# Optimization experiments

Hardware: AMD Instinct MI355X
Metric: run time of the kernel (lower is better)

The kernel has to match this reference:

```python
import jax, jax.numpy as jnp
import numpy as np

D_FEATURES = 64
N_DEPTH = 2048
N_HEAD = 8
N_CHANNEL = 2
N_VCHANNEL = 2
BATCH = 4


def setup_inputs() -> dict:
    key = jax.random.key(0)
    ks = jax.random.split(key, 7)
    F = D_FEATURES
    qk_out = N_HEAD * N_CHANNEL * F   # 1024
    v_out = N_HEAD * N_VCHANNEL * F   # 1024
    # xavier-normal-ish init for expansion (pointwise linear) weights
    def xavier(k, fan_in, fan_out):
        std = float(np.sqrt(2.0 / (fan_in + fan_out)))
        return jax.random.normal(k, (fan_in, fan_out), dtype=jnp.float32) * std
    return {
        "feature_map": jax.random.normal(ks[0], (BATCH, N_DEPTH, F), dtype=jnp.float32),
        "Wq": xavier(ks[1], F, qk_out), "bq": jnp.zeros((qk_out,), jnp.float32),
        "Wk": xavier(ks[2], F, qk_out), "bk": jnp.zeros((qk_out,), jnp.float32),
        "Wv": xavier(ks[3], F, v_out), "bv": jnp.zeros((v_out,), jnp.float32),
        "n_head": N_HEAD,
    }


def _split_heads(x, n_head):
    # [B, D, H*dh] -> [H*B, D, dh]  (matches permute(2,0,1,3).view(H*B, D, -1))
    B, D, HD = x.shape
    dh = HD // n_head
    x = x.reshape(B, D, n_head, dh)
    x = jnp.transpose(x, (2, 0, 1, 3))  # [H, B, D, dh]
    return x.reshape(n_head * B, D, dh)


def reference(feature_map, Wq, bq, Wk, bk, Wv, bv, n_head):
    B, D, F = feature_map.shape
    temperature = jnp.sqrt(jnp.asarray(D, feature_map.dtype))
    # pointwise linear expansion layers
    q = feature_map @ Wq + bq  # [B, D, H*C*F]
    k = feature_map @ Wk + bk
    v = feature_map @ Wv + bv  # [B, D, H*V*F]
    q = _split_heads(q, n_head)  # [H*B, D, C*F]
    k = _split_heads(k, n_head)
    v = _split_heads(v, n_head)  # [H*B, D, V*F]
    # scaled dot production (dropout is identity at inference)
    attn = jnp.einsum('bqd,bkd->bqk', q, k) / temperature  # [H*B, D, D]
    attn = jax.nn.softmax(attn, axis=2)
    out = jnp.einsum('bqk,bkd->bqd', attn, v)  # [H*B, D, V*F]
    # merge heads: [H,B,D,V*F] -> [B,D,H,V*F] -> [B,D,H*V,F] -> [B,H*V,D,F]
    VF = out.shape[-1]
    out = out.reshape(n_head, B, D, VF)
    out = jnp.transpose(out, (1, 2, 0, 3)).reshape(B, D, n_head * (VF // F), F)
    out = jnp.transpose(out, (0, 2, 1, 3))  # [B, H*n_vchannel, D, F]
    return out, attn
```

## Files before the change

kernel.cpp:

```cpp
#include <hip/hip_runtime.h>
#include <hip/hip_bf16.h>

typedef unsigned short ushort_t;
typedef __attribute__((ext_vector_type(8))) short bf16x8;
typedef __attribute__((ext_vector_type(4))) float f32x4;
typedef __attribute__((ext_vector_type(4))) int i32x4;
typedef __attribute__((ext_vector_type(2))) int i32x2;

#define MFMA16(A, B, C) __builtin_amdgcn_mfma_f32_16x16x32_bf16(A, B, C, 0, 0, 0)

static constexpr int BATCH = 4;
static constexpr int DEP = 2048;
static constexpr int NH = 8;
static constexpr int CW = 128;
static constexpr int HBn = 32;
static constexpr float INVTEMP = 0.022097086912079608f;

static __device__ __forceinline__ ushort_t f2bf(float f) {
  __hip_bfloat16 h = __float2bfloat16(f);
  return __builtin_bit_cast(ushort_t, h);
}

__global__ __launch_bounds__(256) void proj_kernel(
    const float* __restrict__ feat,
    const float* __restrict__ Wq, const float* __restrict__ bq,
    const float* __restrict__ Wk, const float* __restrict__ bk,
    const float* __restrict__ Wv, const float* __restrict__ bv,
    ushort_t* __restrict__ q_ws, ushort_t* __restrict__ k_ws,
    ushort_t* __restrict__ vt_ws) {
  const int rt = blockIdx.x;
  const int iw = blockIdx.y >> 2;
  const int ct = blockIdx.y & 3;
  const float* W = (iw == 0) ? Wq : (iw == 1) ? Wk : Wv;
  const float* bs = (iw == 0) ? bq : (iw == 1) ? bk : bv;
  const int tid = threadIdx.x;

  __shared__ float fsm[32 * 64];
  __shared__ ushort_t re[32 * 256];

  {
    const float4* fg = reinterpret_cast<const float4*>(feat + (size_t)rt * 32 * 64);
    float4* fs = reinterpret_cast<float4*>(fsm);
    fs[tid] = fg[tid];
    fs[tid + 256] = fg[tid + 256];
  }
  __syncthreads();

  const int j = ct * 256 + tid;
  float acc[32];
  {
    const float b0 = bs[j];
#pragma unroll
    for (int r = 0; r < 32; ++r) acc[r] = b0;
  }
  for (int f4 = 0; f4 < 16; ++f4) {
    const float w0 = W[(f4 * 4 + 0) * 1024 + j];
    const float w1 = W[(f4 * 4 + 1) * 1024 + j];
    const float w2 = W[(f4 * 4 + 2) * 1024 + j];
    const float w3 = W[(f4 * 4 + 3) * 1024 + j];
#pragma unroll
    for (int r = 0; r < 32; ++r) {
      const float4 fv = *reinterpret_cast<const float4*>(&fsm[r * 64 + f4 * 4]);
      acc[r] = fmaf(fv.x, w0, acc[r]);
      acc[r] = fmaf(fv.y, w1, acc[r]);
      acc[r] = fmaf(fv.z, w2, acc[r]);
      acc[r] = fmaf(fv.w, w3, acc[r]);
    }
  }

  const int b = (rt * 32) >> 11;
  const int d0 = (rt * 32) & 2047;
  if (iw == 2) {
    const int h = j >> 7, cc = j & 127;
    ushort_t us[32];
#pragma unroll
    for (int r = 0; r < 32; ++r) us[r] = f2bf(acc[r]);
    ushort_t* dst = vt_ws + ((size_t)((h * BATCH + b) * CW + cc)) * DEP + d0;
#pragma unroll
    for (int i = 0; i < 4; ++i) {
      unsigned int a0 = us[8 * i + 0] | ((unsigned int)us[8 * i + 1] << 16);
      unsigned int a1 = us[8 * i + 2] | ((unsigned int)us[8 * i + 3] << 16);
      unsigned int a2 = us[8 * i + 4] | ((unsigned int)us[8 * i + 5] << 16);
      unsigned int a3 = us[8 * i + 6] | ((unsigned int)us[8 * i + 7] << 16);
      i32x4 v4 = {(int)a0, (int)a1, (int)a2, (int)a3};
      *reinterpret_cast<i32x4*>(dst + i * 8) = v4;
    }
  } else {
    ushort_t* wsb = (iw == 0) ? q_ws : k_ws;
#pragma unroll
    for (int r = 0; r < 32; ++r) re[r * 256 + tid] = f2bf(acc[r]);
    __syncthreads();
#pragma unroll
    for (int i = 0; i < 4; ++i) {
      const int id = tid + i * 256;
      const int r = id >> 5;
      const int c8 = (id & 31) * 8;
      const int jj = ct * 256 + c8;
      const int hh = jj >> 7, c2 = jj & 127;
      ushort_t* dst = wsb + ((size_t)((hh * BATCH + b) * DEP) + d0 + r) * CW + c2;
      *reinterpret_cast<i32x4*>(dst) = *reinterpret_cast<const i32x4*>(&re[r * 256 + c8]);
    }
  }
}

__global__ __launch_bounds__(256, 2) void attn_kernel(
    const ushort_t* __restrict__ q_ws, const ushort_t* __restrict__ k_ws,
    const ushort_t* __restrict__ vt_ws, float* __restrict__ out,
    float* __restrict__ attn) {
  const int bid = blockIdx.x;
  const int hb = bid >> 4;
  const int qbase = (bid & 15) * 128;
  const int tid = threadIdx.x;
  const int w = tid >> 6;
  const int l = tid & 63;
  const int lg = l >> 4, ll = l & 15;
  const int swz = (ll & 7) << 4;

  __shared__ ushort_t k_lds[64 * 128];
  __shared__ ushort_t v_lds[128 * 64];
  __shared__ ushort_t p_lds[128 * 64];

  bf16x8 qf[2][4];
  const int qw = qbase + 32 * w;
#pragma unroll
  for (int n = 0; n < 2; ++n)
#pragma unroll
    for (int ks = 0; ks < 4; ++ks)
      qf[n][ks] = *reinterpret_cast<const bf16x8*>(
          q_ws + ((size_t)(hb * DEP + qw + 16 * n + ll) * CW + ks * 32 + lg * 8));

  float rs[2] = {0.f, 0.f};

  for (int kt = 0; kt < 32; ++kt) {
    const int ktb = kt * 64;
#pragma unroll
    for (int i = 0; i < 4; ++i) {
      const int id = tid + i * 256;
      const int key = id >> 4, f8 = id & 15;
      i32x4 val = *reinterpret_cast<const i32x4*>(
          k_ws + ((size_t)(hb * DEP + ktb + key) * CW + f8 * 8));
      const int boff = (key * 256 + f8 * 16) ^ ((key & 7) << 4);
      *reinterpret_cast<i32x4*>((char*)k_lds + boff) = val;
    }
    __syncthreads();
    f32x4 accS[4][2];
#pragma unroll
    for (int m = 0; m < 4; ++m)
#pragma unroll
      for (int n = 0; n < 2; ++n) accS[m][n] = (f32x4){0.f, 0.f, 0.f, 0.f};
#pragma unroll
    for (int ks = 0; ks < 4; ++ks) {
      bf16x8 ka[4];
#pragma unroll
      for (int m = 0; m < 4; ++m) {
        const int row = 16 * m + ll;
        const int boff = (row * 256 + ks * 64 + lg * 16) ^ swz;
        ka[m] = *reinterpret_cast<const bf16x8*>((const char*)k_lds + boff);
      }
#pragma unroll
      for (int m = 0; m < 4; ++m)
#pragma unroll
        for (int n = 0; n < 2; ++n) accS[m][n] = MFMA16(ka[m], qf[n][ks], accS[m][n]);
    }
#pragma unroll
    for (int m = 0; m < 4; ++m)
#pragma unroll
      for (int n = 0; n < 2; ++n)
#pragma unroll
        for (int r = 0; r < 4; ++r) rs[n] += __expf(accS[m][n][r] * INVTEMP);
    __syncthreads();
  }
#pragma unroll
  for (int n = 0; n < 2; ++n) {
    rs[n] += __shfl_xor(rs[n], 16);
    rs[n] += __shfl_xor(rs[n], 32);
  }
  const float inv[2] = {1.f / rs[0], 1.f / rs[1]};

  f32x4 accO[8][2];
#pragma unroll
  for (int mc = 0; mc < 8; ++mc)
#pragma unroll
    for (int n = 0; n < 2; ++n) accO[mc][n] = (f32x4){0.f, 0.f, 0.f, 0.f};

  for (int kt = 0; kt < 32; ++kt) {
    const int ktb = kt * 64;
#pragma unroll
    for (int i = 0; i < 4; ++i) {
      const int id = tid + i * 256;
      const int key = id >> 4, f8 = id & 15;
      i32x4 val = *reinterpret_cast<const i32x4*>(
          k_ws + ((size_t)(hb * DEP + ktb + key) * CW + f8 * 8));
      const int boff = (key * 256 + f8 * 16) ^ ((key & 7) << 4);
      *reinterpret_cast<i32x4*>((char*)k_lds + boff) = val;
    }
#pragma unroll
    for (int i = 0; i < 4; ++i) {
      const int id = tid + i * 256;
      const int c = id >> 3, k8 = id & 7;
      i32x4 val = *reinterpret_cast<const i32x4*>(
          vt_ws + ((size_t)(hb * CW + c) * DEP + ktb + k8 * 8));
      const int boff = (c * 128 + k8 * 16) ^ ((c & 7) << 4);
      *reinterpret_cast<i32x4*>((char*)v_lds + boff) = val;
    }
    __syncthreads();

    f32x4 accS[4][2];
#pragma unroll
    for (int m = 0; m < 4; ++m)
#pragma unroll
      for (int n = 0; n < 2; ++n) accS[m][n] = (f32x4){0.f, 0.f, 0.f, 0.f};
#pragma unroll
    for (int ks = 0; ks < 4; ++ks) {
      bf16x8 ka[4];
#pragma unroll
      for (int m = 0; m < 4; ++m) {
        const int row = 16 * m + ll;
        const int boff = (row * 256 + ks * 64 + lg * 16) ^ swz;
        ka[m] = *reinterpret_cast<const bf16x8*>((const char*)k_lds + boff);
      }
#pragma unroll
      for (int m = 0; m < 4; ++m)
#pragma unroll
        for (int n = 0; n < 2; ++n) accS[m][n] = MFMA16(ka[m], qf[n][ks], accS[m][n]);
    }

#pragma unroll
    for (int m = 0; m < 4; ++m)
#pragma unroll
      for (int n = 0; n < 2; ++n) {
        f32x4 p;
#pragma unroll
        for (int r = 0; r < 4; ++r) p[r] = __expf(accS[m][n][r] * INVTEMP) * inv[n];
        const int q = qw + 16 * n + ll;
        const int key = ktb + 16 * m + 4 * lg;
        *reinterpret_cast<f32x4*>(attn + (size_t)hb * DEP * DEP + (size_t)q * DEP + key) = p;
        unsigned int lo = f2bf(p[0]) | ((unsigned int)f2bf(p[1]) << 16);
        unsigned int hi = f2bf(p[2]) | ((unsigned int)f2bf(p[3]) << 16);
        i32x2 pw = {(int)lo, (int)hi};
        const int boff = ((32 * w + 16 * n + ll) * 128 + (16 * m + 4 * lg) * 2) ^ swz;
        *reinterpret_cast<i32x2*>((char*)p_lds + boff) = pw;
      }

#pragma unroll
    for (int kk = 0; kk < 2; ++kk) {
      bf16x8 pb[2];
#pragma unroll
      for (int n = 0; n < 2; ++n) {
        const int boff = ((32 * w + 16 * n + ll) * 128 + (kk * 32 + lg * 8) * 2) ^ swz;
        pb[n] = *reinterpret_cast<const bf16x8*>((const char*)p_lds + boff);
      }
#pragma unroll
      for (int mc = 0; mc < 8; ++mc) {
        const int boff = ((16 * mc + ll) * 128 + (kk * 32 + lg * 8) * 2) ^ swz;
        bf16x8 va = *reinterpret_cast<const bf16x8*>((const char*)v_lds + boff);
#pragma unroll
        for (int n = 0; n < 2; ++n) accO[mc][n] = MFMA16(va, pb[n], accO[mc][n]);
      }
    }
    __syncthreads();
  }

  const int hh = hb >> 2, b = hb & 3;
#pragma unroll
  for (int mc = 0; mc < 8; ++mc)
#pragma unroll
    for (int n = 0; n < 2; ++n) {
      const int c0 = 16 * mc + 4 * lg;
      const int qg = qbase + 32 * w + 16 * n + ll;
      float* dst = out + (((size_t)(b * 16 + hh * 2 + (c0 >> 6)) * DEP + qg) * 64 + (c0 & 63));
      *reinterpret_cast<f32x4*>(dst) = accO[mc][n];
    }
}

extern "C" void kernel_launch(void* const* d_in, const int* in_sizes, int n_in,
                              void* d_out, int out_size, void* d_ws, size_t ws_size,
                              hipStream_t stream) {
  const float* feat = (const float*)d_in[0];
  const float* Wq = (const float*)d_in[1];
  const float* bq = (const float*)d_in[2];
  const float* Wk = (const float*)d_in[3];
  const float* bk = (const float*)d_in[4];
  const float* Wv = (const float*)d_in[5];
  const float* bv = (const float*)d_in[6];

  ushort_t* q_ws = (ushort_t*)d_ws;
  ushort_t* k_ws = q_ws + (size_t)HBn * DEP * CW;
  ushort_t* vt_ws = k_ws + (size_t)HBn * DEP * CW;

  float* out = (float*)d_out;
  float* attn = out + (size_t)BATCH * 16 * DEP * 64;

  hipLaunchKernelGGL(proj_kernel, dim3(256, 12), dim3(256), 0, stream,
                     feat, Wq, bq, Wk, bk, Wv, bv, q_ws, k_ws, vt_ws);
  hipLaunchKernelGGL(attn_kernel, dim3(512), dim3(256), 0, stream,
                     q_ws, k_ws, vt_ws, out, attn);
}
```

Baseline: 291.7 us.

## Cache full unnormalized probability rows in LDS to avoid recomputing QK^T

The attention kernel now computes QK^T once per 32-query block and stores the unnormalized bf16 exp values for whole 2048-key rows in about 128KB of dynamic LDS. A second pass reads them back to run the PV MFMAs and to write the normalized attn matrix, instead of recomputing scores. The softmax scale and log2e are folded into Q in the projection kernel so that exp2 can be used directly. K and V are now read straight from global memory rather than staged through LDS, and the grid is remapped to 2048 blocks of 512 threads. The attn output is now rounded from bf16 probabilities, which costs precision, and the large LDS footprint limits occupancy.

```diff
diff --git a/kernel.cpp b/kernel.cpp
--- a/kernel.cpp
+++ b/kernel.cpp
@@ -9,16 +9,30 @@
 
 #define MFMA16(A, B, C) __builtin_amdgcn_mfma_f32_16x16x32_bf16(A, B, C, 0, 0, 0)
 
+#if defined(__has_builtin)
+#if __has_builtin(__builtin_amdgcn_exp2f)
+#define EXP2(x) __builtin_amdgcn_exp2f(x)
+#else
+#define EXP2(x) exp2f(x)
+#endif
+#else
+#define EXP2(x) exp2f(x)
+#endif
+
 static constexpr int BATCH = 4;
 static constexpr int DEP = 2048;
 static constexpr int NH = 8;
 static constexpr int CW = 128;
 static constexpr int HBn = 32;
-static constexpr float INVTEMP = 0.022097086912079608f;
+static constexpr float QSCALE = (float)(1.4426950408889634 / 45.254833995939045);
 
 static __device__ __forceinline__ ushort_t f2bf(float f) {
   __hip_bfloat16 h = __float2bfloat16(f);
   return __builtin_bit_cast(ushort_t, h);
+}
+static __device__ __forceinline__ float bf2f(ushort_t u) {
+  unsigned int v = ((unsigned int)u) << 16;
+  return __builtin_bit_cast(float, v);
 }
 
 __global__ __launch_bounds__(256) void proj_kernel(
@@ -67,6 +81,10 @@
       acc[r] = fmaf(fv.w, w3, acc[r]);
     }
   }
+  if (iw == 0) {
+#pragma unroll
+    for (int r = 0; r < 32; ++r) acc[r] *= QSCALE;
+  }
 
   const int b = (rt * 32) >> 11;
   const int d0 = (rt * 32) & 2047;
@@ -103,174 +121,110 @@
   }
 }
 
-__global__ __launch_bounds__(256, 2) void attn_kernel(
+__global__ __launch_bounds__(512, 2) void attn_kernel(
     const ushort_t* __restrict__ q_ws, const ushort_t* __restrict__ k_ws,
     const ushort_t* __restrict__ vt_ws, float* __restrict__ out,
     float* __restrict__ attn) {
-  const int bid = blockIdx.x;
-  const int hb = bid >> 4;
-  const int qbase = (bid & 15) * 128;
+  extern __shared__ char smem[];
+  float* rsbuf = (float*)(smem + 131072);
+  float* invbuf = rsbuf + 128;
+
+  const int bid0 = blockIdx.x;
+  const int wg = (bid0 & 7) * 256 + (bid0 >> 3);
+  const int hb = wg >> 6;
+  const int qbase = (wg & 63) * 32;
+
   const int tid = threadIdx.x;
-  const int w = tid >> 6;
-  const int l = tid & 63;
+  const int w = tid >> 6, l = tid & 63;
   const int lg = l >> 4, ll = l & 15;
-  const int swz = (ll & 7) << 4;
-
-  __shared__ ushort_t k_lds[64 * 128];
-  __shared__ ushort_t v_lds[128 * 64];
-  __shared__ ushort_t p_lds[128 * 64];
-
-  bf16x8 qf[2][4];
-  const int qw = qbase + 32 * w;
-#pragma unroll
-  for (int n = 0; n < 2; ++n)
+
+  const int kw = w & 3, qh = w >> 2;
+  bf16x8 qf[4];
+  {
+    const ushort_t* qrow =
+        q_ws + ((size_t)(hb * DEP + qbase + 16 * qh + ll)) * CW + lg * 8;
 #pragma unroll
     for (int ks = 0; ks < 4; ++ks)
-      qf[n][ks] = *reinterpret_cast<const bf16x8*>(
-          q_ws + ((size_t)(hb * DEP + qw + 16 * n + ll) * CW + ks * 32 + lg * 8));
-
-  float rs[2] = {0.f, 0.f};
-
+      qf[ks] = *reinterpret_cast<const bf16x8*>(qrow + ks * 32);
+  }
+  const int qloc = 16 * qh + ll;
+  const int pswz = (qloc & 7) << 4;
+  float rs = 0.f;
+  const ushort_t* kb0 = k_ws + (size_t)hb * DEP * CW + (size_t)(16 * kw + ll) * CW + lg * 8;
   for (int kt = 0; kt < 32; ++kt) {
-    const int ktb = kt * 64;
-#pragma unroll
-    for (int i = 0; i < 4; ++i) {
-      const int id = tid + i * 256;
-      const int key = id >> 4, f8 = id & 15;
-      i32x4 val = *reinterpret_cast<const i32x4*>(
-          k_ws + ((size_t)(hb * DEP + ktb + key) * CW + f8 * 8));
-      const int boff = (key * 256 + f8 * 16) ^ ((key & 7) << 4);
-      *reinterpret_cast<i32x4*>((char*)k_lds + boff) = val;
-    }
-    __syncthreads();
-    f32x4 accS[4][2];
-#pragma unroll
-    for (int m = 0; m < 4; ++m)
-#pragma unroll
-      for (int n = 0; n < 2; ++n) accS[m][n] = (f32x4){0.f, 0.f, 0.f, 0.f};
-#pragma unroll
-    for (int ks = 0; ks < 4; ++ks) {
-      bf16x8 ka[4];
-#pragma unroll
-      for (int m = 0; m < 4; ++m) {
-        const int row = 16 * m + ll;
-        const int boff = (row * 256 + ks * 64 + lg * 16) ^ swz;
-        ka[m] = *reinterpret_cast<const bf16x8*>((const char*)k_lds + boff);
+    const ushort_t* krow = kb0 + (size_t)kt * 64 * CW;
+    bf16x8 ka[4];
+#pragma unroll
+    for (int ks = 0; ks < 4; ++ks)
+      ka[ks] = *reinterpret_cast<const bf16x8*>(krow + ks * 32);
+    f32x4 acc = {0.f, 0.f, 0.f, 0.f};
+#pragma unroll
+    for (int ks = 0; ks < 4; ++ks) acc = MFMA16(ka[ks], qf[ks], acc);
+    float pv0 = EXP2(acc[0]), pv1 = EXP2(acc[1]);
+    float pv2 = EXP2(acc[2]), pv3 = EXP2(acc[3]);
+    rs += (pv0 + pv1) + (pv2 + pv3);
+    unsigned int lo = f2bf(pv0) | ((unsigned int)f2bf(pv1) << 16);
+    unsigned int hi = f2bf(pv2) | ((unsigned int)f2bf(pv3) << 16);
+    const int key = kt * 64 + 16 * kw + 4 * lg;
+    const int boff = (qloc * 4096 + key * 2) ^ pswz;
+    *reinterpret_cast<i32x2*>(smem + boff) = i32x2{(int)lo, (int)hi};
+  }
+  rs += __shfl_xor(rs, 16);
+  rs += __shfl_xor(rs, 32);
+  if (lg == 0) rsbuf[kw * 32 + qloc] = rs;
+  __syncthreads();
+  if (tid < 32)
+    invbuf[tid] = 1.f / ((rsbuf[tid] + rsbuf[32 + tid]) + (rsbuf[64 + tid] + rsbuf[96 + tid]));
+  __syncthreads();
+
+  const int cp = w >> 1, qhb = w & 1;
+  const int qloc2 = 16 * qhb + ll;
+  const int pswz2 = (qloc2 & 7) << 4;
+  const int qA = tid >> 4;
+  const float invA = invbuf[qA];
+  float* attnrow = attn + (size_t)hb * DEP * DEP + (size_t)(qbase + qA) * DEP;
+  const ushort_t* vb0 = vt_ws + (size_t)hb * CW * DEP;
+
+  f32x4 accO[2] = {{0.f, 0.f, 0.f, 0.f}, {0.f, 0.f, 0.f, 0.f}};
+  for (int kt = 0; kt < 32; ++kt) {
+#pragma unroll
+    for (int ks2 = 0; ks2 < 2; ++ks2) {
+      const int kb = kt * 64 + ks2 * 32 + lg * 8;
+      const int boff = (qloc2 * 4096 + kb * 2) ^ pswz2;
+      bf16x8 pb = *reinterpret_cast<const bf16x8*>(smem + boff);
+#pragma unroll
+      for (int i = 0; i < 2; ++i) {
+        const int c = 16 * (2 * cp + i) + ll;
+        bf16x8 va = *reinterpret_cast<const bf16x8*>(vb0 + (size_t)c * DEP + kb);
+        accO[i] = MFMA16(va, pb, accO[i]);
       }
-#pragma unroll
-      for (int m = 0; m < 4; ++m)
-#pragma unroll
-        for (int n = 0; n < 2; ++n) accS[m][n] = MFMA16(ka[m], qf[n][ks], accS[m][n]);
-    }
-#pragma unroll
-    for (int m = 0; m < 4; ++m)
-#pragma unroll
-      for (int n = 0; n < 2; ++n)
-#pragma unroll
-        for (int r = 0; r < 4; ++r) rs[n] += __expf(accS[m][n][r] * INVTEMP);
-    __syncthreads();
-  }
-#pragma unroll
-  for (int n = 0; n < 2; ++n) {
-    rs[n] += __shfl_xor(rs[n], 16);
-    rs[n] += __shfl_xor(rs[n], 32);
-  }
-  const float inv[2] = {1.f / rs[0], 1.f / rs[1]};
-
-  f32x4 accO[8][2];
-#pragma unroll
-  for (int mc = 0; mc < 8; ++mc)
-#pragma unroll
-    for (int n = 0; n < 2; ++n) accO[mc][n] = (f32x4){0.f, 0.f, 0.f, 0.f};
-
-  for (int kt = 0; kt < 32; ++kt) {
-    const int ktb = kt * 64;
-#pragma unroll
-    for (int i = 0; i < 4; ++i) {
-      const int id = tid + i * 256;
-      const int key = id >> 4, f8 = id & 15;
-      i32x4 val = *reinterpret_cast<const i32x4*>(
-          k_ws + ((size_t)(hb * DEP + ktb + key) * CW + f8 * 8));
-      const int boff = (key * 256 + f8 * 16) ^ ((key & 7) << 4);
-      *reinterpret_cast<i32x4*>((char*)k_lds + boff) = val;
-    }
-#pragma unroll
-    for (int i = 0; i < 4; ++i) {
-      const int id = tid + i * 256;
-      const int c = id >> 3, k8 = id & 7;
-      i32x4 val = *reinterpret_cast<const i32x4*>(
-          vt_ws + ((size_t)(hb * CW + c) * DEP + ktb + k8 * 8));
-      const int boff = (c * 128 + k8 * 16) ^ ((c & 7) << 4);
-      *reinterpret_cast<i32x4*>((char*)v_lds + boff) = val;
-    }
-    __syncthreads();
-
-    f32x4 accS[4][2];
-#pragma unroll
-    for (int m = 0; m < 4; ++m)
-#pragma unroll
-      for (int n = 0; n < 2; ++n) accS[m][n] = (f32x4){0.f, 0.f, 0.f, 0.f};
-#pragma unroll
-    for (int ks = 0; ks < 4; ++ks) {
-      bf16x8 ka[4];
-#pragma unroll
-      for (int m = 0; m < 4; ++m) {
-        const int row = 16 * m + ll;
-        const int boff = (row * 256 + ks * 64 + lg * 16) ^ swz;
-        ka[m] = *reinterpret_cast<const bf16x8*>((const char*)k_lds + boff);
+    }
+    if ((kt & 1) == 0) {
+      const int key8 = kt * 64 + (tid & 15) * 8;
+      const int boff = (qA * 4096 + key8 * 2) ^ ((qA & 7) << 4);
+      bf16x8 pr = *reinterpret_cast<const bf16x8*>(smem + boff);
+      f32x4 s0, s1;
+#pragma unroll
+      for (int r = 0; r < 4; ++r) {
+        s0[r] = bf2f((ushort_t)pr[r]) * invA;
+        s1[r] = bf2f((ushort_t)pr[r + 4]) * invA;
       }
-#pragma unroll
-      for (int m = 0; m < 4; ++m)
-#pragma unroll
-        for (int n = 0; n < 2; ++n) accS[m][n] = MFMA16(ka[m], qf[n][ks], accS[m][n]);
-    }
-
-#pragma unroll
-    for (int m = 0; m < 4; ++m)
-#pragma unroll
-      for (int n = 0; n < 2; ++n) {
-        f32x4 p;
-#pragma unroll
-        for (int r = 0; r < 4; ++r) p[r] = __expf(accS[m][n][r] * INVTEMP) * inv[n];
-        const int q = qw + 16 * n + ll;
-        const int key = ktb + 16 * m + 4 * lg;
-        *reinterpret_cast<f32x4*>(attn + (size_t)hb * DEP * DEP + (size_t)q * DEP + key) = p;
-        unsigned int lo = f2bf(p[0]) | ((unsigned int)f2bf(p[1]) << 16);
-        unsigned int hi = f2bf(p[2]) | ((unsigned int)f2bf(p[3]) << 16);
-        i32x2 pw = {(int)lo, (int)hi};
-        const int boff = ((32 * w + 16 * n + ll) * 128 + (16 * m + 4 * lg) * 2) ^ swz;
-        *reinterpret_cast<i32x2*>((char*)p_lds + boff) = pw;
-      }
-
-#pragma unroll
-    for (int kk = 0; kk < 2; ++kk) {
-      bf16x8 pb[2];
-#pragma unroll
-      for (int n = 0; n < 2; ++n) {
-        const int boff = ((32 * w + 16 * n + ll) * 128 + (kk * 32 + lg * 8) * 2) ^ swz;
-        pb[n] = *reinterpret_cast<const bf16x8*>((const char*)p_lds + boff);
-      }
-#pragma unroll
-      for (int mc = 0; mc < 8; ++mc) {
-        const int boff = ((16 * mc + ll) * 128 + (kk * 32 + lg * 8) * 2) ^ swz;
-        bf16x8 va = *reinterpret_cast<const bf16x8*>((const char*)v_lds + boff);
-#pragma unroll
-        for (int n = 0; n < 2; ++n) accO[mc][n] = MFMA16(va, pb[n], accO[mc][n]);
-      }
-    }
-    __syncthreads();
+      *reinterpret_cast<f32x4*>(attnrow + key8) = s0;
+      *reinterpret_cast<f32x4*>(attnrow + key8 + 4) = s1;
+    }
   }
 
   const int hh = hb >> 2, b = hb & 3;
-#pragma unroll
-  for (int mc = 0; mc < 8; ++mc)
-#pragma unroll
-    for (int n = 0; n < 2; ++n) {
-      const int c0 = 16 * mc + 4 * lg;
-      const int qg = qbase + 32 * w + 16 * n + ll;
-      float* dst = out + (((size_t)(b * 16 + hh * 2 + (c0 >> 6)) * DEP + qg) * 64 + (c0 & 63));
-      *reinterpret_cast<f32x4*>(dst) = accO[mc][n];
-    }
+  const float invO = invbuf[qloc2];
+#pragma unroll
+  for (int i = 0; i < 2; ++i) {
+    const int c0 = 16 * (2 * cp + i) + 4 * lg;
+    f32x4 r;
+#pragma unroll
+    for (int r4 = 0; r4 < 4; ++r4) r[r4] = accO[i][r4] * invO;
+    float* dst = out + ((size_t)(b * 16 + hh * 2 + (c0 >> 6)) * DEP + qbase + qloc2) * 64 + (c0 & 63);
+    *reinterpret_cast<f32x4*>(dst) = r;
+  }
 }
 
 extern "C" void kernel_launch(void* const* d_in, const int* in_sizes, int n_in,
@@ -291,8 +245,15 @@
   float* out = (float*)d_out;
   float* attn = out + (size_t)BATCH * 16 * DEP * 64;
 
+  static int smem_attr_set = 0;
+  if (!smem_attr_set) {
+    (void)hipFuncSetAttribute((const void*)attn_kernel,
+                              hipFuncAttributeMaxDynamicSharedMemorySize, 131712);
+    smem_attr_set = 1;
+  }
+
   hipLaunchKernelGGL(proj_kernel, dim3(256, 12), dim3(256), 0, stream,
                      feat, Wq, bq, Wk, bk, Wv, bv, q_ws, k_ws, vt_ws);
-  hipLaunchKernelGGL(attn_kernel, dim3(512), dim3(256), 0, stream,
+  hipLaunchKernelGGL(attn_kernel, dim3(2048), dim3(512), 131712, stream,
                      q_ws, k_ws, vt_ws, out, attn);
 }
```

New measurement: 612.8 us. 110% more time.
